# Kernel tuning notes

Measured on AMD Instinct MI355X. Metric: run time of the kernel, lower is better.

Reference implementation:

```python
import jax, jax.numpy as jnp
import numpy as np

EMB = 768
HEADS = 8
HEAD_DIM = EMB // HEADS  # 96


def setup_inputs() -> dict:
    key = jax.random.key(0)
    ks = jax.random.split(key, 5)
    B, N = 4, 2048
    x = jax.random.normal(ks[0], (B, N, EMB), dtype=jnp.float32)
    s_in = 1.0 / np.sqrt(EMB)
    # weights stored as (in, out); equivalent to torch Linear y = x @ W + b
    w_qkv = jax.random.normal(ks[1], (EMB, 3 * EMB), dtype=jnp.float32) * s_in
    b_qkv = jax.random.normal(ks[2], (3 * EMB,), dtype=jnp.float32) * 0.02
    w_proj = jax.random.normal(ks[3], (EMB, EMB), dtype=jnp.float32) * s_in
    b_proj = jax.random.normal(ks[4], (EMB,), dtype=jnp.float32) * 0.02
    return {"x": x, "w_qkv": w_qkv, "b_qkv": b_qkv, "w_proj": w_proj, "b_proj": b_proj}


def reference(x, w_qkv, b_qkv, w_proj, b_proj):
    B, N, _ = x.shape
    qkv = x @ w_qkv + b_qkv  # [B, N, 3*EMB]
    # rearrange 'b n (h d qkv) -> qkv b h n d': qkv is the innermost split axis
    qkv = qkv.reshape(B, N, HEADS, HEAD_DIM, 3)
    qkv = jnp.transpose(qkv, (4, 0, 2, 1, 3))  # [3, B, H, N, D]
    q, k, v = qkv[0], qkv[1], qkv[2]
    inv_scale = 1.0 / np.sqrt(HEAD_DIM)  # applied AFTER softmax (faithful to source)
    scores = jnp.einsum('bhqd,bhkd->bhqk', q, k)
    attn = jax.nn.softmax(scores, axis=-1) * inv_scale
    out = jnp.einsum('bhqk,bhkd->bhqd', attn, v)
    out = jnp.transpose(out, (0, 2, 1, 3)).reshape(B, N, EMB)  # b h n d -> b n (h d)
    return out @ w_proj + b_proj
```

## Files before the change

### kernel.cpp

```cpp
#include <hip/hip_runtime.h>
#include <hip/hip_bf16.h>

#define EMB 768
#define NHEADS 8
#define HDIM 96
#define SEQ 2048
#define BATCH 4
#define QKV_COLS 2304
#define PB ((size_t)SEQ * EMB)

typedef _Float16 f16;
typedef _Float16 f16x8 __attribute__((ext_vector_type(8)));
typedef float f32x4 __attribute__((ext_vector_type(4)));

__device__ __forceinline__ void gl_lds16(const f16* g, f16* l) {
  __builtin_amdgcn_global_load_lds((const __attribute__((address_space(1))) void*)g,
                                   (__attribute__((address_space(3))) void*)l, 16, 0, 0);
}
__device__ __forceinline__ f32x4 shflx4(f32x4 v, int m) {
  f32x4 r;
  r[0] = __shfl_xor(v[0], m); r[1] = __shfl_xor(v[1], m);
  r[2] = __shfl_xor(v[2], m); r[3] = __shfl_xor(v[3], m);
  return r;
}
__device__ __forceinline__ f32x4 vmax4(f32x4 a, f32x4 b) {
  f32x4 r;
  r[0] = fmaxf(a[0], b[0]); r[1] = fmaxf(a[1], b[1]);
  r[2] = fmaxf(a[2], b[2]); r[3] = fmaxf(a[3], b[3]);
  return r;
}

__global__ __launch_bounds__(256) void conv_x8_k(const float* __restrict__ in, size_t in_off,
                                                 f16* __restrict__ out, int n8) {
  int i = blockIdx.x * 256 + threadIdx.x;
  if (i >= n8) return;
  const float4 a = *(const float4*)(in + in_off + (size_t)i * 8);
  const float4 b = *(const float4*)(in + in_off + (size_t)i * 8 + 4);
  f16x8 o;
  o[0] = (f16)a.x; o[1] = (f16)a.y; o[2] = (f16)a.z; o[3] = (f16)a.w;
  o[4] = (f16)b.x; o[5] = (f16)b.y; o[6] = (f16)b.z; o[7] = (f16)b.w;
  *(f16x8*)(out + (size_t)i * 8) = o;
}

__global__ __launch_bounds__(256) void wqkv_perm_k(const float* __restrict__ in,
                                                   f16* __restrict__ out) {
  int t = blockIdx.x * 256 + threadIdx.x;
  if (t >= QKV_COLS * (EMB / 8)) return;
  const int colp = t / (EMB / 8);
  const int r8 = (t - colp * (EMB / 8)) * 8;
  const int s = colp / 768, rem = colp - s * 768;
  const int h = rem / 96, d = rem - h * 96;
  const int c = h * 288 + d * 3 + s;
  f16x8 o;
#pragma unroll
  for (int i = 0; i < 8; i++) o[i] = (f16)in[(size_t)(r8 + i) * QKV_COLS + c];
  *(f16x8*)(out + (size_t)colp * EMB + r8) = o;
}

__global__ __launch_bounds__(256) void wproj_t_k(const float* __restrict__ in,
                                                 f16* __restrict__ out) {
  int t = blockIdx.x * 256 + threadIdx.x;
  if (t >= EMB * (EMB / 8)) return;
  const int cp = t / (EMB / 8);
  const int r8 = (t - cp * (EMB / 8)) * 8;
  f16x8 o;
#pragma unroll
  for (int i = 0; i < 8; i++) o[i] = (f16)in[(size_t)(r8 + i) * EMB + cp];
  *(f16x8*)(out + (size_t)cp * EMB + r8) = o;
}

__global__ __launch_bounds__(256) void bias_perm_k(const float* __restrict__ bq_in,
                                                   float* __restrict__ bq_out,
                                                   const float* __restrict__ bp_in,
                                                   float* __restrict__ bp_out) {
  int i = blockIdx.x * 256 + threadIdx.x;
  if (i < QKV_COLS) {
    const int s = i / 768, rem = i - s * 768;
    const int h = rem / 96, d = rem - h * 96;
    bq_out[i] = bq_in[h * 288 + d * 3 + s];
  }
  if (i < EMB) bp_out[i] = bp_in[i];
}

template<int MODE>
__global__ __launch_bounds__(256) void gemm_bt(
    const f16* __restrict__ A, const f16* __restrict__ Bt,
    const float* __restrict__ bias, float* __restrict__ Cout,
    f16* __restrict__ QK, f16* __restrict__ Vt,
    int M, int N, int Kd)
{
  __shared__ f16 smem[MODE == 1 ? 17408 : 8192];
  f16* sA = smem;
  f16* sB = smem + 4096;
  const int tid  = threadIdx.x;
  const int wave = tid >> 6, lane = tid & 63;
  const int quad = lane >> 4, l16 = lane & 15;
  const int tile_m = blockIdx.y * 128, tile_n = blockIdx.x * 128;
  const int wm = (wave >> 1) * 64, wn = (wave & 1) * 64;

  f32x4 acc[4][4];
  for (int i = 0; i < 4; i++)
    for (int j = 0; j < 4; j++)
      acc[i][j] = f32x4{0.f, 0.f, 0.f, 0.f};

  for (int k0 = 0; k0 < Kd; k0 += 32) {
    __syncthreads();
#pragma unroll
    for (int it = 0; it < 2; it++) {
      const int ch  = (it * 4 + wave) * 64 + lane;
      const int row = ch >> 2, c8 = (ch & 3) * 8;
      if (MODE == 2) {
        const int grow = tile_m + row;
        const int bb = grow >> 11, n = grow & 2047;
        const int hh = k0 / 96, d0 = k0 - hh * 96 + c8;
        gl_lds16(A + ((size_t)(bb * NHEADS + hh) * SEQ + n) * HDIM + d0,
                 &sA[(it * 4 + wave) * 512]);
      } else {
        gl_lds16(A + (size_t)(tile_m + row) * Kd + k0 + c8, &sA[(it * 4 + wave) * 512]);
      }
      gl_lds16(Bt + (size_t)(tile_n + row) * Kd + k0 + c8, &sB[(it * 4 + wave) * 512]);
    }
    __syncthreads();

    f16x8 af[4], bfr[4];
    for (int i = 0; i < 4; i++) af[i]  = *(const f16x8*)&sA[(wm + i * 16 + l16) * 32 + quad * 8];
    for (int j = 0; j < 4; j++) bfr[j] = *(const f16x8*)&sB[(wn + j * 16 + l16) * 32 + quad * 8];
    for (int i = 0; i < 4; i++)
      for (int j = 0; j < 4; j++)
        acc[i][j] = __builtin_amdgcn_mfma_f32_16x16x32_f16(af[i], bfr[j], acc[i][j], 0, 0, 0);
  }

  if (MODE == 1 && tile_n >= 1536) {
    __syncthreads();
    f16* sT = smem;
    for (int j = 0; j < 4; j++) {
      const int cl = wn + j * 16 + l16;
      const float bv = bias[tile_n + cl];
      for (int i = 0; i < 4; i++)
        for (int r = 0; r < 4; r++)
          sT[cl * 136 + wm + i * 16 + quad * 4 + r] = (f16)(acc[i][j][r] + bv);
    }
    __syncthreads();
    const int bb = tile_m >> 11;
    const int n0 = tile_m & 2047;
#pragma unroll
    for (int l = 0; l < 8; l++) {
      const int cc = l * 256 + tid;
      const int rh = cc >> 4, nof = (cc & 15) * 8;
      const int hd = (tile_n - 1536) + rh;
      const int h = hd / 96, d = hd - h * 96;
      f16x8 v = *(const f16x8*)&sT[rh * 136 + nof];
      *(f16x8*)(Vt + ((size_t)(bb * NHEADS + h) * HDIM + d) * SEQ + n0 + nof) = v;
    }
  } else {
    for (int j = 0; j < 4; j++) {
      const int col = tile_n + wn + j * 16 + l16;
      const float bv = bias[col];
      for (int i = 0; i < 4; i++) {
        for (int r = 0; r < 4; r++) {
          const int row = tile_m + wm + i * 16 + quad * 4 + r;
          const float fv = acc[i][j][r] + bv;
          if (MODE != 1) Cout[(size_t)row * N + col] = fv;
          else           QK  [(size_t)row * 1536 + col] = (f16)fv;
        }
      }
    }
  }
}

__global__ __launch_bounds__(256, 2) void attn_k(
    const f16* __restrict__ QK, const f16* __restrict__ Vt,
    f16* __restrict__ Out , int nbh)
{
  __shared__ f16 sK[128 * 96];
  __shared__ f16 sV[96 * 128];
  __shared__ f16 sP[128 * 64];
  const int tid  = threadIdx.x;
  const int wave = tid >> 6, lane = tid & 63;
  const int quad = lane >> 4, l16 = lane & 15;

  const int bid = blockIdx.x;
  const int xcd = bid & 7, idx = bid >> 3;
  const int bh  = xcd * (nbh >> 3) + (idx >> 4);
  const int qt  = idx & 15;
  const int b = bh >> 3, h = bh & 7;

  const int wrow = wave * 32;

  const f16* Qb = QK + (size_t)(b * SEQ + qt * 128 + wrow) * 1536 + h * 96;
  const f16* Kb = QK + (size_t)(b * SEQ) * 1536 + 768 + h * 96;
  const f16* Vb = Vt + (size_t)bh * HDIM * SEQ;

  int koff[6], voff[6];
#pragma unroll
  for (int i = 0; i < 6; i++) {
    const int ck = i * 256 + tid;
    const int krow = ck / 12, pu = ck - krow * 12;
    const int u = (pu + 12 - krow % 12) % 12;
    koff[i] = krow * 1536 + u * 8;
    const int vd = ck >> 4, pv = ck & 15;
    voff[i] = vd * SEQ + (pv ^ (vd & 15)) * 8;
  }

  f16x8 qf[2][3];
#pragma unroll
  for (int ti = 0; ti < 2; ti++)
#pragma unroll
    for (int kc = 0; kc < 3; kc++)
      qf[ti][kc] = *(const f16x8*)(Qb + (size_t)(ti * 16 + l16) * 1536 + kc * 32 + quad * 8);

  f32x4 oacc[2][6];
#pragma unroll
  for (int ti = 0; ti < 2; ti++)
#pragma unroll
    for (int dj = 0; dj < 6; dj++)
      oacc[ti][dj] = f32x4{0.f, 0.f, 0.f, 0.f};
  f32x4 m_run[2], l_run[2];
#pragma unroll
  for (int ti = 0; ti < 2; ti++) {
    m_run[ti] = f32x4{-1e30f, -1e30f, -1e30f, -1e30f};
    l_run[ti] = f32x4{0.f, 0.f, 0.f, 0.f};
  }

  {
#pragma unroll
    for (int i = 0; i < 6; i++) gl_lds16(Kb + koff[i], &sK[(i * 256 + wave * 64) * 8]);
#pragma unroll
    for (int i = 0; i < 6; i++) gl_lds16(Vb + voff[i], &sV[(i * 256 + wave * 64) * 8]);
  }

  const int NT = SEQ / 128;
  for (int kt = 0; kt < NT; kt++) {
    if (kt == 0) asm volatile("s_waitcnt vmcnt(0)" ::: "memory");
    else         asm volatile("s_waitcnt vmcnt(6)" ::: "memory");
    __builtin_amdgcn_s_barrier();
    __builtin_amdgcn_sched_barrier(0);

    f32x4 sacc[2][8];
#pragma unroll
    for (int ti = 0; ti < 2; ti++)
#pragma unroll
      for (int j = 0; j < 8; j++)
        sacc[ti][j] = f32x4{0.f, 0.f, 0.f, 0.f};
#pragma unroll
    for (int kc = 0; kc < 3; kc++) {
#pragma unroll
      for (int j = 0; j < 8; j++) {
        const int krow = j * 16 + l16;
        const f16x8 kf = *(const f16x8*)&sK[krow * 96 + ((kc * 4 + quad + krow) % 12) * 8];
        sacc[0][j] = __builtin_amdgcn_mfma_f32_16x16x32_f16(qf[0][kc], kf, sacc[0][j], 0, 0, 0);
        sacc[1][j] = __builtin_amdgcn_mfma_f32_16x16x32_f16(qf[1][kc], kf, sacc[1][j], 0, 0, 0);
      }
    }

    __builtin_amdgcn_sched_barrier(0);
    __builtin_amdgcn_s_barrier();
    if (kt < NT - 1) {
      const f16* kb = Kb + (size_t)((kt + 1) * 128) * 1536;
#pragma unroll
      for (int i = 0; i < 6; i++) gl_lds16(kb + koff[i], &sK[(i * 256 + wave * 64) * 8]);
    }
    __builtin_amdgcn_sched_barrier(0);

    f32x4 rsv[2];
#pragma unroll
    for (int ti = 0; ti < 2; ti++) {
      f32x4 vmx = sacc[ti][0];
#pragma unroll
      for (int j = 1; j < 8; j++) vmx = vmax4(vmx, sacc[ti][j]);
      const int ok = __all(vmx[0] <= m_run[ti][0] + 8.f &&
                           vmx[1] <= m_run[ti][1] + 8.f &&
                           vmx[2] <= m_run[ti][2] + 8.f &&
                           vmx[3] <= m_run[ti][3] + 8.f);
      if (!ok) {
        for (int m = 1; m < 16; m <<= 1) vmx = vmax4(vmx, shflx4(vmx, m));
        const f32x4 nm = vmax4(m_run[ti], vmx);
        f32x4 alpha;
        alpha[0] = __expf(m_run[ti][0] - nm[0]); alpha[1] = __expf(m_run[ti][1] - nm[1]);
        alpha[2] = __expf(m_run[ti][2] - nm[2]); alpha[3] = __expf(m_run[ti][3] - nm[3]);
        m_run[ti] = nm;
        l_run[ti] *= alpha;
#pragma unroll
        for (int dj = 0; dj < 6; dj++) oacc[ti][dj] *= alpha;
      }
      rsv[ti] = f32x4{0.f, 0.f, 0.f, 0.f};
    }

    if (kt < NT - 1) asm volatile("s_waitcnt vmcnt(6)" ::: "memory");
    else             asm volatile("s_waitcnt vmcnt(0)" ::: "memory");
    __builtin_amdgcn_s_barrier();
    __builtin_amdgcn_sched_barrier(0);

#pragma unroll
    for (int c2 = 0; c2 < 2; c2++) {
#pragma unroll
      for (int ti = 0; ti < 2; ti++) {
        const int prow = wrow + ti * 16 + quad * 4;
#pragma unroll
        for (int jl = 0; jl < 4; jl++) {
          const int j = c2 * 4 + jl;
          f32x4 p;
          p[0] = __expf(sacc[ti][j][0] - m_run[ti][0]);
          p[1] = __expf(sacc[ti][j][1] - m_run[ti][1]);
          p[2] = __expf(sacc[ti][j][2] - m_run[ti][2]);
          p[3] = __expf(sacc[ti][j][3] - m_run[ti][3]);
          rsv[ti] += p;
          const int unit = jl * 2 + (l16 >> 3);
          const int within = l16 & 7;
#pragma unroll
          for (int rr = 0; rr < 4; rr++) {
            const int row = prow + rr;
            sP[row * 64 + (unit ^ (row & 7)) * 8 + within] = (f16)p[rr];
          }
        }
      }
#pragma unroll
      for (int kc2 = 0; kc2 < 2; kc2++) {
        const f16x8 pf0 = *(const f16x8*)&sP[(wrow + l16) * 64
                                            + ((kc2 * 4 + quad) ^ (l16 & 7)) * 8];
        const f16x8 pf1 = *(const f16x8*)&sP[(wrow + 16 + l16) * 64
                                            + ((kc2 * 4 + quad) ^ (l16 & 7)) * 8];
#pragma unroll
        for (int dj = 0; dj < 6; dj++) {
          const int vph = (c2 * 8 + kc2 * 4 + quad) ^ l16;
          const f16x8 vf = *(const f16x8*)&sV[(dj * 16 + l16) * 128 + vph * 8];
          oacc[0][dj] = __builtin_amdgcn_mfma_f32_16x16x32_f16(pf0, vf, oacc[0][dj], 0, 0, 0);
          oacc[1][dj] = __builtin_amdgcn_mfma_f32_16x16x32_f16(pf1, vf, oacc[1][dj], 0, 0, 0);
        }
      }
    }

    __builtin_amdgcn_sched_barrier(0);
    __builtin_amdgcn_s_barrier();
    if (kt < NT - 1) {
      const f16* vb = Vb + (kt + 1) * 128;
#pragma unroll
      for (int i = 0; i < 6; i++) gl_lds16(vb + voff[i], &sV[(i * 256 + wave * 64) * 8]);
    }
    __builtin_amdgcn_sched_barrier(0);

#pragma unroll
    for (int ti = 0; ti < 2; ti++) l_run[ti] += rsv[ti];
  }

#pragma unroll
  for (int ti = 0; ti < 2; ti++)
    for (int m = 1; m < 16; m <<= 1) l_run[ti] += shflx4(l_run[ti], m);

  const float inv_scale = 0.10206207261596577f;
#pragma unroll
  for (int ti = 0; ti < 2; ti++) {
#pragma unroll
    for (int r = 0; r < 4; r++) {
      const int qrow = qt * 128 + wrow + ti * 16 + quad * 4 + r;
      const float invl = inv_scale / l_run[ti][r];
      const size_t base = ((size_t)bh * SEQ + qrow) * HDIM;
#pragma unroll
      for (int dj = 0; dj < 6; dj++)
        Out[base + dj * 16 + l16] = (f16)(oacc[ti][dj][r] * invl);
    }
  }
}

extern "C" void kernel_launch(void* const* d_in, const int* in_sizes, int n_in,
                              void* d_out, int out_size, void* d_ws, size_t ws_size,
                              hipStream_t stream) {
  const float* x      = (const float*)d_in[0];
  const float* w_qkv  = (const float*)d_in[1];
  const float* b_qkv  = (const float*)d_in[2];
  const float* w_proj = (const float*)d_in[3];
  const float* b_proj = (const float*)d_in[4];
  float* outF = (float*)d_out;

  const size_t fixed = 256 + (size_t)QKV_COLS * EMB * 2 + (size_t)EMB * EMB * 2
                     + QKV_COLS * 4 + EMB * 4 + 256;
  const size_t perb = (size_t)4 * PB * 2;
  int nb = (ws_size >= fixed + 4 * perb) ? 4 : (ws_size >= fixed + 2 * perb) ? 2 : 1;

  char* ws = (char*)d_ws;
  ws += 256;
  f16*   wqkvT  = (f16*)ws;   ws += (size_t)QKV_COLS * EMB * 2;
  f16*   wprojT = (f16*)ws;   ws += (size_t)EMB * EMB * 2;
  float* bq     = (float*)ws; ws += (size_t)QKV_COLS * 4;
  float* bp     = (float*)ws; ws += (size_t)EMB * 4 + 256;
  f16* QK   = (f16*)ws;       ws += (size_t)nb * 2 * PB * 2;
  f16* Vt   = (f16*)ws;       ws += (size_t)nb * PB * 2;
  f16* attn = (f16*)ws;       ws += (size_t)nb * PB * 2;

  wqkv_perm_k<<<(QKV_COLS * (EMB / 8) + 255) / 256, 256, 0, stream>>>(w_qkv, wqkvT);
  wproj_t_k<<<(EMB * (EMB / 8) + 255) / 256, 256, 0, stream>>>(w_proj, wprojT);
  bias_perm_k<<<(QKV_COLS + 255) / 256, 256, 0, stream>>>(b_qkv, bq, b_proj, bp);

  for (int outer = 0; outer < BATCH / nb; outer++) {
    const int bbase = outer * nb;
    const size_t goff = (size_t)bbase * PB;
    f16* xg = (f16*)(outF + goff);
    const int n8 = (int)((size_t)nb * PB / 8);
    conv_x8_k<<<(n8 + 255) / 256, 256, 0, stream>>>(x, goff, xg, n8);

    dim3 g1(QKV_COLS / 128, nb * SEQ / 128);
    gemm_bt<1><<<g1, 256, 0, stream>>>(xg, wqkvT, bq, nullptr, QK, Vt,
                                       nb * SEQ, QKV_COLS, EMB);

    attn_k<<<dim3(16 * nb * NHEADS), 256, 0, stream>>>(QK, Vt, attn, nb * NHEADS);

    dim3 g3(EMB / 128, nb * SEQ / 128);
    gemm_bt<2><<<g3, 256, 0, stream>>>(attn, wprojT, bp, outF + goff,
                                       nullptr, nullptr,
                                       nb * SEQ, EMB, EMB);
  }
}
```

Baseline: 305.4 us.

## Merge weight prep into one LDS-tiled transpose kernel and remap GEMM tiles for XCDs

Replaces three weight/bias preprocessing kernels with a single kernel that transposes weights through a 32x33 shared-memory tile, so global reads and writes are coalesced instead of strided column gathers. It also saves two launches. The GEMM kernels now remap the linear workgroup index so that consecutive tiles land on the same XCD chunk, aiming for better L2 reuse of A/B tiles across the eight dies. The transpose writes are now 2-byte scattered stores per column, and the swizzle only applies when the grid size is divisible by 8.

New measurement: 290.4 us. 4.9% less time.

```diff
diff --git a/kernel.cpp b/kernel.cpp
--- a/kernel.cpp
+++ b/kernel.cpp
@@ -42,44 +42,41 @@
   *(f16x8*)(out + (size_t)i * 8) = o;
 }
 
-__global__ __launch_bounds__(256) void wqkv_perm_k(const float* __restrict__ in,
-                                                   f16* __restrict__ out) {
-  int t = blockIdx.x * 256 + threadIdx.x;
-  if (t >= QKV_COLS * (EMB / 8)) return;
-  const int colp = t / (EMB / 8);
-  const int r8 = (t - colp * (EMB / 8)) * 8;
-  const int s = colp / 768, rem = colp - s * 768;
-  const int h = rem / 96, d = rem - h * 96;
-  const int c = h * 288 + d * 3 + s;
-  f16x8 o;
-#pragma unroll
-  for (int i = 0; i < 8; i++) o[i] = (f16)in[(size_t)(r8 + i) * QKV_COLS + c];
-  *(f16x8*)(out + (size_t)colp * EMB + r8) = o;
-}
-
-__global__ __launch_bounds__(256) void wproj_t_k(const float* __restrict__ in,
-                                                 f16* __restrict__ out) {
-  int t = blockIdx.x * 256 + threadIdx.x;
-  if (t >= EMB * (EMB / 8)) return;
-  const int cp = t / (EMB / 8);
-  const int r8 = (t - cp * (EMB / 8)) * 8;
-  f16x8 o;
-#pragma unroll
-  for (int i = 0; i < 8; i++) o[i] = (f16)in[(size_t)(r8 + i) * EMB + cp];
-  *(f16x8*)(out + (size_t)cp * EMB + r8) = o;
-}
-
-__global__ __launch_bounds__(256) void bias_perm_k(const float* __restrict__ bq_in,
-                                                   float* __restrict__ bq_out,
-                                                   const float* __restrict__ bp_in,
-                                                   float* __restrict__ bp_out) {
-  int i = blockIdx.x * 256 + threadIdx.x;
-  if (i < QKV_COLS) {
-    const int s = i / 768, rem = i - s * 768;
-    const int h = rem / 96, d = rem - h * 96;
-    bq_out[i] = bq_in[h * 288 + d * 3 + s];
-  }
-  if (i < EMB) bp_out[i] = bp_in[i];
+__global__ __launch_bounds__(256) void pre_k(
+    const float* __restrict__ wq, f16* __restrict__ wqT,
+    const float* __restrict__ wp, f16* __restrict__ wpT,
+    const float* __restrict__ bq_in, float* __restrict__ bq_out,
+    const float* __restrict__ bp_in, float* __restrict__ bp_out)
+{
+  __shared__ float t[32][33];
+  const int bid = blockIdx.x;
+  const int tx = threadIdx.x & 31, ty = threadIdx.x >> 5;
+  if (bid < 1728 + 576) {
+    const float* in; f16* out; int C, ct, rt; bool qkv;
+    if (bid < 1728) { in = wq; out = wqT; C = QKV_COLS;
+                      ct = (bid % 72) * 32; rt = (bid / 72) * 32; qkv = true; }
+    else            { const int b2 = bid - 1728; in = wp; out = wpT; C = EMB;
+                      ct = (b2 % 24) * 32; rt = (b2 / 24) * 32; qkv = false; }
+#pragma unroll
+    for (int p = 0; p < 4; p++)
+      t[p * 8 + ty][tx] = in[(size_t)(rt + p * 8 + ty) * C + ct + tx];
+    __syncthreads();
+#pragma unroll
+    for (int p = 0; p < 4; p++) {
+      const int c = ct + p * 8 + ty;
+      int colp;
+      if (qkv) { const int h = c / 288, rem = c - h * 288, d = rem / 3, s = rem - d * 3;
+                 colp = s * 768 + h * 96 + d; }
+      else     colp = c;
+      out[(size_t)colp * EMB + rt + tx] = (f16)t[tx][p * 8 + ty];
+    }
+  } else {
+    for (int i = threadIdx.x; i < QKV_COLS; i += 256) {
+      const int s = i / 768, rem = i - s * 768, h = rem / 96, d = rem - h * 96;
+      bq_out[i] = bq_in[h * 288 + d * 3 + s];
+    }
+    for (int i = threadIdx.x; i < EMB; i += 256) bp_out[i] = bp_in[i];
+  }
 }
 
 template<int MODE>
@@ -95,7 +92,15 @@
   const int tid  = threadIdx.x;
   const int wave = tid >> 6, lane = tid & 63;
   const int quad = lane >> 4, l16 = lane & 15;
-  const int tile_m = blockIdx.y * 128, tile_n = blockIdx.x * 128;
+  int lin = blockIdx.y * gridDim.x + blockIdx.x;
+  {
+    const int nwg = gridDim.x * gridDim.y;
+    if ((nwg & 7) == 0) {
+      const int chunk = nwg >> 3;
+      lin = (lin & 7) * chunk + (lin >> 3);
+    }
+  }
+  const int tile_m = (lin / gridDim.x) * 128, tile_n = (lin % gridDim.x) * 128;
   const int wm = (wave >> 1) * 64, wn = (wave & 1) * 64;
 
   f32x4 acc[4][4];
@@ -387,9 +392,8 @@
   f16* Vt   = (f16*)ws;       ws += (size_t)nb * PB * 2;
   f16* attn = (f16*)ws;       ws += (size_t)nb * PB * 2;
 
-  wqkv_perm_k<<<(QKV_COLS * (EMB / 8) + 255) / 256, 256, 0, stream>>>(w_qkv, wqkvT);
-  wproj_t_k<<<(EMB * (EMB / 8) + 255) / 256, 256, 0, stream>>>(w_proj, wprojT);
-  bias_perm_k<<<(QKV_COLS + 255) / 256, 256, 0, stream>>>(b_qkv, bq, b_proj, bp);
+  pre_k<<<1728 + 576 + 1, 256, 0, stream>>>(w_qkv, wqkvT, w_proj, wprojT,
+                                            b_qkv, bq, b_proj, bp);
 
   for (int outer = 0; outer < BATCH / nb; outer++) {
     const int bbase = outer * nb;
```
